# Kernel tuning notes

Hardware: AMD Instinct MI355X
Metric: run time of the kernel (lower is better)

## Reference

```python
import jax, jax.numpy as jnp
import numpy as np

HEADS = 16
NEG_INF = -1e30


def rel_shift(t):
    # t: [b, h, i, j] with i == j; Transformer-XL style relative shift
    b, h, i, j = t.shape
    t = jnp.pad(t, ((0, 0), (0, 0), (0, 0), (1, 0)))  # zero pad on last dim front
    t = t.reshape(b, h, j + 1, i)[:, :, 1:]
    return t.reshape(b, h, i, j)


def setup_inputs() -> dict:
    key = jax.random.key(0)
    ks = jax.random.split(key, 8)
    b, n, dim = 2, 2048, 1024
    d_head = dim // HEADS
    w = 0.02
    return {
        "x": jax.random.normal(ks[0], (b, n, dim), dtype=jnp.float32),
        "pos_emb": jax.random.normal(ks[1], (n, dim), dtype=jnp.float32),
        "Wq": jax.random.normal(ks[2], (dim, dim), dtype=jnp.float32) * w,
        "bq": jnp.zeros((dim,), dtype=jnp.float32),
        "Wkv": jax.random.normal(ks[3], (dim, 2 * dim), dtype=jnp.float32) * w,
        "bkv": jnp.zeros((2 * dim,), dtype=jnp.float32),
        "Wp": jax.random.normal(ks[4], (dim, d_head), dtype=jnp.float32) * w,
        "bp": jnp.zeros((d_head,), dtype=jnp.float32),
        "Wo": jax.random.normal(ks[5], (dim, dim), dtype=jnp.float32) * w,
        "bo": jnp.zeros((dim,), dtype=jnp.float32),
    }


def reference(x, pos_emb, Wq, bq, Wkv, bkv, Wp, bp, Wo, bo):
    b, n, dim = x.shape
    h = HEADS
    d = dim // h
    scale = d ** -0.5

    q = (x @ Wq + bq).reshape(b, n, h, d).transpose(0, 2, 1, 3)  # b h n d
    kv = x @ Wkv + bkv
    k, v = jnp.split(kv, 2, axis=-1)
    k = k.reshape(b, n, h, d).transpose(0, 2, 1, 3)
    v = v.reshape(b, n, h, d).transpose(0, 2, 1, 3)

    dots = jnp.einsum('bhid,bhjd->bhij', q, k) * scale

    # relative position bias
    p = pos_emb @ Wp + bp  # [n, d]
    pos_attn = jnp.einsum('bhid,jd->bhij', q, p) * scale
    dots = dots + rel_shift(pos_attn)

    # causal mask
    causal = jnp.triu(jnp.ones((n, n), dtype=bool), 1)
    dots = jnp.where(causal[None, None], NEG_INF, dots)

    attn = jax.nn.softmax(dots, axis=-1)
    out = jnp.einsum('bhij,bhjd->bhid', attn, v)
    out = out.transpose(0, 2, 1, 3).reshape(b, n, dim)
    return out @ Wo + bo
```

## Files before the change

kernel.cpp:

```cpp
#include <hip/hip_runtime.h>
#include <hip/hip_bf16.h>
#include <cstdint>
#include <cstddef>

#define SEQ_N 2048
#define DIM   1024
#define NHEAD 16
#define DH    64

typedef __bf16 bf16;
typedef __attribute__((ext_vector_type(8))) __bf16 bf16x8;
typedef __attribute__((ext_vector_type(4))) __bf16 bf16x4;
typedef __attribute__((ext_vector_type(4))) float f32x4;

__device__ __forceinline__ void gl_lds16(const bf16* g, bf16* l) {
    __builtin_amdgcn_global_load_lds(
        (const __attribute__((address_space(1))) unsigned int*)g,
        (__attribute__((address_space(3))) unsigned int*)l, 16, 0, 0);
}

__global__ __launch_bounds__(256) void prep_kernel(
    const float* __restrict__ x, const float* __restrict__ pos,
    const float* __restrict__ Wq, const float* __restrict__ Wkv,
    const float* __restrict__ Wo, const float* __restrict__ Wp,
    bf16* __restrict__ xb, bf16* __restrict__ posb,
    bf16* __restrict__ WqkvT, bf16* __restrict__ WoT, bf16* __restrict__ WpT)
{
    int bid = blockIdx.x;
    if (bid < 6144) {
        const int NX = 4096 * 1024;
        int i = (bid * 256 + threadIdx.x) * 4;
        if (i < NX) {
            float4 v = *(const float4*)&x[i];
            xb[i + 0] = (bf16)v.x; xb[i + 1] = (bf16)v.y;
            xb[i + 2] = (bf16)v.z; xb[i + 3] = (bf16)v.w;
        } else {
            int j = i - NX;
            float4 v = *(const float4*)&pos[j];
            posb[j + 0] = (bf16)v.x; posb[j + 1] = (bf16)v.y;
            posb[j + 2] = (bf16)v.z; posb[j + 3] = (bf16)v.w;
        }
        return;
    }
    __shared__ float t[32][33];
    bid -= 6144;
    const float* src; bf16* dst; int tidx, nx, N;
    if (bid < 1024)      { src = Wq;  dst = WqkvT;                       tidx = bid;        nx = 32; N = 1024; }
    else if (bid < 3072) { src = Wkv; dst = WqkvT + (size_t)1024 * 1024; tidx = bid - 1024; nx = 64; N = 2048; }
    else if (bid < 4096) { src = Wo;  dst = WoT;                         tidx = bid - 3072; nx = 32; N = 1024; }
    else                 { src = Wp;  dst = WpT;                         tidx = bid - 4096; nx = 2;  N = 64;   }
    int n0 = (tidx % nx) * 32, k0 = (tidx / nx) * 32;
    int tx = threadIdx.x & 31, ty = threadIdx.x >> 5;
    #pragma unroll
    for (int r = ty; r < 32; r += 8)
        t[r][tx] = src[(size_t)(k0 + r) * N + n0 + tx];
    __syncthreads();
    #pragma unroll
    for (int r = ty; r < 32; r += 8)
        dst[(size_t)(n0 + r) * 1024 + k0 + tx] = (bf16)t[tx][r];
}

__global__ __launch_bounds__(256) void qkvp_kernel(
    const bf16* __restrict__ xb, const bf16* __restrict__ WqkvT,
    const bf16* __restrict__ posb, const bf16* __restrict__ WpT,
    const float* __restrict__ bq, const float* __restrict__ bkv,
    const float* __restrict__ bp,
    bf16* __restrict__ qbuf, bf16* __restrict__ kbuf,
    bf16* __restrict__ vtbuf, bf16* __restrict__ pfrag)
{
    __shared__ __align__(16) bf16 sm[128 * 132];
    bf16* At = sm;
    bf16* Bt = sm + 128 * 64;
    const int tid = threadIdx.x, w = tid >> 6, lane = tid & 63;
    const int q = lane >> 4, ln15 = lane & 15;
    const int lr = lane >> 3, c_log = (lane & 7) ^ lr;
    const int bx = blockIdx.x, by = blockIdx.y;
    const int m0 = by * 128;

    if (bx == 24) {
        if (by >= 16) return;
        f32x4 acc[2][4] = {};
        for (int k0 = 0; k0 < 1024; k0 += 64) {
            __syncthreads();
            #pragma unroll
            for (int t = 0; t < 4; ++t)
                gl_lds16(&posb[(size_t)(m0 + 32 * w + 8 * t + lr) * 1024 + k0 + c_log * 8],
                         &At[(32 * w + 8 * t) * 64]);
            #pragma unroll
            for (int t = 0; t < 2; ++t)
                gl_lds16(&WpT[(size_t)(16 * w + 8 * t + lr) * 1024 + k0 + c_log * 8],
                         &Bt[(16 * w + 8 * t) * 64]);
            __syncthreads();
            bf16x8 bfr[2][4];
            #pragma unroll
            for (int ks = 0; ks < 2; ++ks)
                #pragma unroll
                for (int sn = 0; sn < 4; ++sn) {
                    int rb = 16 * sn + ln15;
                    bfr[ks][sn] = *(const bf16x8*)&Bt[(rb * 8 + ((4 * ks + q) ^ (rb & 7))) * 8];
                }
            #pragma unroll
            for (int sm2 = 0; sm2 < 2; ++sm2) {
                int ra = 32 * w + 16 * sm2 + ln15;
                #pragma unroll
                for (int ks = 0; ks < 2; ++ks) {
                    bf16x8 af = *(const bf16x8*)&At[(ra * 8 + ((4 * ks + q) ^ (ra & 7))) * 8];
                    #pragma unroll
                    for (int sn = 0; sn < 4; ++sn)
                        acc[sm2][sn] = __builtin_amdgcn_mfma_f32_16x16x32_bf16(
                            af, bfr[ks][sn], acc[sm2][sn], 0, 0, 0);
                }
            }
        }
        #pragma unroll
        for (int sm2 = 0; sm2 < 2; ++sm2)
            #pragma unroll
            for (int sn = 0; sn < 4; ++sn)
                #pragma unroll
                for (int r = 0; r < 4; ++r) {
                    int row = m0 + 32 * w + 16 * sm2 + 4 * q + r;
                    int d = 16 * sn + ln15;
                    int sb = row >> 4, lnp = row & 15;
                    int ks2 = d >> 5, qd = (d >> 3) & 3, e = d & 7;
                    pfrag[(((size_t)sb * 2 + ks2) * 64 + qd * 16 + lnp) * 8 + e] =
                        (bf16)(acc[sm2][sn][r] + bp[d]);
                }
        return;
    }

    const int n0 = bx * 128;
    const int wm = w >> 1, wn = w & 1;
    f32x4 acc[4][4] = {};

    for (int k0 = 0; k0 < 1024; k0 += 64) {
        __syncthreads();
        #pragma unroll
        for (int t = 0; t < 4; ++t) {
            int r = 32 * w + 8 * t + lr;
            gl_lds16(&xb[(size_t)(m0 + r) * 1024 + k0 + c_log * 8],
                     &At[(32 * w + 8 * t) * 64]);
            gl_lds16(&WqkvT[(size_t)(n0 + r) * 1024 + k0 + c_log * 8],
                     &Bt[(32 * w + 8 * t) * 64]);
        }
        __syncthreads();

        bf16x8 af[2][4], bfr[2][4];
        #pragma unroll
        for (int ks = 0; ks < 2; ++ks)
            #pragma unroll
            for (int s = 0; s < 4; ++s) {
                int ra = 64 * wm + 16 * s + ln15;
                af[ks][s]  = *(const bf16x8*)&At[(ra * 8 + ((4 * ks + q) ^ (ra & 7))) * 8];
                int rb = 64 * wn + 16 * s + ln15;
                bfr[ks][s] = *(const bf16x8*)&Bt[(rb * 8 + ((4 * ks + q) ^ (rb & 7))) * 8];
            }
        #pragma unroll
        for (int ks = 0; ks < 2; ++ks)
            #pragma unroll
            for (int si = 0; si < 4; ++si)
                #pragma unroll
                for (int sj = 0; sj < 4; ++sj)
                    acc[si][sj] = __builtin_amdgcn_mfma_f32_16x16x32_bf16(
                        af[ks][si], bfr[ks][sj], acc[si][sj], 0, 0, 0);
    }

    if (bx < 16) {
        #pragma unroll
        for (int si = 0; si < 4; ++si)
            #pragma unroll
            for (int sj = 0; sj < 4; ++sj)
                #pragma unroll
                for (int r = 0; r < 4; ++r) {
                    int row = m0 + 64 * wm + 16 * si + 4 * q + r;
                    int col = n0 + 64 * wn + 16 * sj + ln15;
                    float v = acc[si][sj][r] + (col < 1024 ? bq[col] : bkv[col - 1024]);
                    if (col < 1024) qbuf[(size_t)row * 1024 + col] = (bf16)v;
                    else            kbuf[(size_t)row * 1024 + (col - 1024)] = (bf16)v;
                }
    } else {
        __syncthreads();
        #pragma unroll
        for (int si = 0; si < 4; ++si)
            #pragma unroll
            for (int sj = 0; sj < 4; ++sj) {
                int dL = 64 * wn + 16 * sj + ln15;
                int tL = 64 * wm + 16 * si + 4 * q;
                float bias = bkv[1024 + (bx - 16) * 128 + dL];
                bf16x4 o4;
                #pragma unroll
                for (int r = 0; r < 4; ++r)
                    o4[r] = (bf16)(acc[si][sj][r] + bias);
                *(bf16x4*)&sm[dL * 132 + tL] = o4;
            }
        __syncthreads();
        const int b = m0 >> 11;
        const int t0 = m0 & 2047;
        const int h0 = (bx - 16) * 2;
        #pragma unroll
        for (int p = 0; p < 16; ++p) {
            int d = (tid >> 5) + 8 * p;
            int t = (tid & 31) * 4;
            bf16x4 v4 = *(const bf16x4*)&sm[d * 132 + t];
            int rowv = (b * NHEAD + h0 + (d >> 6)) * DH + (d & 63);
            *(bf16x4*)&vtbuf[(size_t)rowv * SEQ_N + t0 + t] = v4;
        }
    }
}

__global__ __launch_bounds__(256, 4) void attn_mfma_kernel(
    const bf16* __restrict__ qb,
    const bf16* __restrict__ kb,
    const bf16* __restrict__ vt,
    const bf16* __restrict__ pfrag,
    bf16* __restrict__ ob)
{
    const int f    = (int)blockIdx.x + ((int)blockIdx.y << 5);
    const int slot = f >> 3;
    const int bh   = ((f & 7) << 2) + (slot & 3);
    const int bi   = bh >> 4, hh = bh & 15;
    const int g    = (slot >> 2) & 7;
    const int pass = slot >> 5;
    const int qblk = (pass == 0) ? g
                   : (pass == 1) ? 15 - g
                   : (pass == 2) ? 16 + g
                   :               31 - g;
    const int i0 = qblk << 6;
    const int tid = threadIdx.x, w = tid >> 6, lane = tid & 63;
    const int q = lane >> 4, ln15 = lane & 15;
    const int lr = lane >> 3, c_log = (lane & 7) ^ lr;

    __shared__ __align__(16) bf16 smem[17664];
    bf16* Qs  = smem;
    bf16* S2L = smem + w * 1344;
    bf16* Ks  = smem + 5376;
    bf16* Vs  = smem + 9472;
    bf16* Pw  = smem + 13568 + w * 1024;

    const bf16* qbase = qb + ((size_t)(bi * SEQ_N + i0)) * DIM + hh * DH;
    const bf16* kbase = kb + ((size_t)bi * SEQ_N) * DIM + hh * DH;
    const bf16* vbase = vt + ((size_t)(bi * NHEAD + hh) * DH) * SEQ_N;

    #pragma unroll
    for (int t = 0; t < 2; ++t)
        gl_lds16(qbase + (size_t)(16 * w + 8 * t + lr) * DIM + c_log * 8,
                 &Qs[(16 * w + 8 * t) * 64]);
    __syncthreads();
    bf16x8 qf0, qf1;
    {
        int rq = 16 * w + ln15;
        qf0 = *(const bf16x8*)&Qs[(rq * 8 + ((q    ) ^ (rq & 7))) * 8];
        qf1 = *(const bf16x8*)&Qs[(rq * 8 + ((4 + q) ^ (rq & 7))) * 8];
    }
    __syncthreads();

    const int A0 = 127 - 4 * qblk - w;
    f32x4 s2r4;
    {
        bf16x8 f0 = *(const bf16x8*)&pfrag[(((size_t)A0 * 2 + 0) * 64 + lane) * 8];
        bf16x8 f1 = *(const bf16x8*)&pfrag[(((size_t)A0 * 2 + 1) * 64 + lane) * 8];
        f32x4 a = {0.f, 0.f, 0.f, 0.f};
        a = __builtin_amdgcn_mfma_f32_16x16x32_bf16(f0, qf0, a, 0, 0, 0);
        a = __builtin_amdgcn_mfma_f32_16x16x32_bf16(f1, qf1, a, 0, 0, 0);
        s2r4 = a;
    }

    float m_run = -1e30f, l_run = 0.f;
    f32x4 O_T[4] = {};

    for (int jt = 0; jt <= qblk; ++jt) {
        const int j0 = jt << 6;

        bf16x8 pfA[4][2];
        #pragma unroll
        for (int s = 1; s <= 4; ++s) {
            int sb = A0 + 4 * jt + s;
            if (sb > 127) sb = 127;
            pfA[s-1][0] = *(const bf16x8*)&pfrag[(((size_t)sb * 2 + 0) * 64 + lane) * 8];
            pfA[s-1][1] = *(const bf16x8*)&pfrag[(((size_t)sb * 2 + 1) * 64 + lane) * 8];
        }
        #pragma unroll
        for (int t = 0; t < 2; ++t) {
            int r = 16 * w + 8 * t + lr;
            gl_lds16(kbase + (size_t)(j0 + r) * DIM + c_log * 8,
                     &Ks[(16 * w + 8 * t) * 64]);
            gl_lds16(vbase + (size_t)r * SEQ_N + j0 + c_log * 8,
                     &Vs[(16 * w + 8 * t) * 64]);
        }

        f32x4 s2r[5];
        s2r[0] = s2r4;
        #pragma unroll
        for (int s = 1; s <= 4; ++s) {
            f32x4 a = {0.f, 0.f, 0.f, 0.f};
            a = __builtin_amdgcn_mfma_f32_16x16x32_bf16(pfA[s-1][0], qf0, a, 0, 0, 0);
            a = __builtin_amdgcn_mfma_f32_16x16x32_bf16(pfA[s-1][1], qf1, a, 0, 0, 0);
            s2r[s] = a;
        }
        s2r4 = s2r[4];
        #pragma unroll
        for (int s = 0; s < 5; ++s)
            #pragma unroll
            for (int r = 0; r < 4; ++r)
                S2L[ln15 * 84 + 16 * s + 4 * q + r] = (bf16)s2r[s][r];

        __syncthreads();

        float sv[4][4];
        #pragma unroll
        for (int sn = 0; sn < 4; ++sn) {
            int rk = 16 * sn + ln15;
            bf16x8 k0f = *(const bf16x8*)&Ks[(rk * 8 + ((q    ) ^ (rk & 7))) * 8];
            bf16x8 k1f = *(const bf16x8*)&Ks[(rk * 8 + ((4 + q) ^ (rk & 7))) * 8];
            f32x4 a = {0.f, 0.f, 0.f, 0.f};
            a = __builtin_amdgcn_mfma_f32_16x16x32_bf16(k0f, qf0, a, 0, 0, 0);
            a = __builtin_amdgcn_mfma_f32_16x16x32_bf16(k1f, qf1, a, 0, 0, 0);
            #pragma unroll
            for (int r = 0; r < 4; ++r) {
                int jl = 16 * sn + 4 * q + r;
                float b = (float)S2L[ln15 * 84 + 15 - ln15 + jl];
                sv[sn][r] = (a[r] + b) * 0.125f;
            }
        }
        if (jt == qblk) {
            #pragma unroll
            for (int sn = 0; sn < 4; ++sn)
                #pragma unroll
                for (int r = 0; r < 4; ++r)
                    if (16 * sn + 4 * q + r > 16 * w + ln15)
                        sv[sn][r] = -1e30f;
        }

        float mx = sv[0][0];
        #pragma unroll
        for (int sn = 0; sn < 4; ++sn)
            #pragma unroll
            for (int r = 0; r < 4; ++r)
                mx = fmaxf(mx, sv[sn][r]);
        mx = fmaxf(mx, __shfl_xor(mx, 16));
        mx = fmaxf(mx, __shfl_xor(mx, 32));
        const float mn = fmaxf(m_run, mx);
        float sum = 0.f;
        #pragma unroll
        for (int sn = 0; sn < 4; ++sn)
            #pragma unroll
            for (int r = 0; r < 4; ++r) {
                float e = __expf(sv[sn][r] - mn);
                sv[sn][r] = e;
                sum += e;
            }
        sum += __shfl_xor(sum, 16);
        sum += __shfl_xor(sum, 32);
        const float alpha = __expf(m_run - mn);
        l_run = l_run * alpha + sum;
        m_run = mn;

        #pragma unroll
        for (int sn = 0; sn < 4; ++sn)
            #pragma unroll
            for (int r = 0; r < 4; ++r) {
                int chunk = (2 * sn + (q >> 1)) ^ (ln15 & 7);
                Pw[ln15 * 64 + chunk * 8 + 4 * (q & 1) + r] = (bf16)sv[sn][r];
            }
        #pragma unroll
        for (int sd = 0; sd < 4; ++sd)
            #pragma unroll
            for (int r = 0; r < 4; ++r)
                O_T[sd][r] *= alpha;

        __builtin_amdgcn_s_waitcnt(0);

        #pragma unroll
        for (int ks = 0; ks < 2; ++ks) {
            bf16x8 pT = *(const bf16x8*)&Pw[ln15 * 64 + (((4 * ks + q) ^ (ln15 & 7))) * 8];
            #pragma unroll
            for (int sd = 0; sd < 4; ++sd) {
                int rv = 16 * sd + ln15;
                bf16x8 vf = *(const bf16x8*)&Vs[(rv * 8 + ((4 * ks + q) ^ (rv & 7))) * 8];
                O_T[sd] = __builtin_amdgcn_mfma_f32_16x16x32_bf16(vf, pT, O_T[sd], 0, 0, 0);
            }
        }
        __syncthreads();
    }

    const float inv = 1.0f / l_run;
    const size_t row = (size_t)bi * SEQ_N + i0 + 16 * w + ln15;
    #pragma unroll
    for (int sd = 0; sd < 4; ++sd) {
        bf16x4 o4;
        #pragma unroll
        for (int r = 0; r < 4; ++r)
            o4[r] = (bf16)(O_T[sd][r] * inv);
        *(bf16x4*)&ob[row * DIM + hh * DH + 16 * sd + 4 * q] = o4;
    }
}

__global__ __launch_bounds__(256) void outproj_kernel(
    const bf16* __restrict__ ab, const bf16* __restrict__ WoT,
    const float* __restrict__ bo, float* __restrict__ out)
{
    __shared__ __align__(16) bf16 At[128 * 64];
    __shared__ __align__(16) bf16 Bt[64 * 64];
    const int tid = threadIdx.x, w = tid >> 6, lane = tid & 63;
    const int q = lane >> 4, ln15 = lane & 15;
    const int lr = lane >> 3, c_log = (lane & 7) ^ lr;
    const int m0 = blockIdx.y * 128, n0 = blockIdx.x * 64;

    f32x4 acc[2][4] = {};
    for (int k0 = 0; k0 < 1024; k0 += 64) {
        __syncthreads();
        #pragma unroll
        for (int t = 0; t < 4; ++t)
            gl_lds16(&ab[(size_t)(m0 + 32 * w + 8 * t + lr) * 1024 + k0 + c_log * 8],
                     &At[(32 * w + 8 * t) * 64]);
        #pragma unroll
        for (int t = 0; t < 2; ++t)
            gl_lds16(&WoT[(size_t)(n0 + 16 * w + 8 * t + lr) * 1024 + k0 + c_log * 8],
                     &Bt[(16 * w + 8 * t) * 64]);
        __syncthreads();

        bf16x8 bfr[2][4];
        #pragma unroll
        for (int ks = 0; ks < 2; ++ks)
            #pragma unroll
            for (int sn = 0; sn < 4; ++sn) {
                int rb = 16 * sn + ln15;
                bfr[ks][sn] = *(const bf16x8*)&Bt[(rb * 8 + ((4 * ks + q) ^ (rb & 7))) * 8];
            }
        #pragma unroll
        for (int sm2 = 0; sm2 < 2; ++sm2) {
            int ra = 32 * w + 16 * sm2 + ln15;
            #pragma unroll
            for (int ks = 0; ks < 2; ++ks) {
                bf16x8 af = *(const bf16x8*)&At[(ra * 8 + ((4 * ks + q) ^ (ra & 7))) * 8];
                #pragma unroll
                for (int sn = 0; sn < 4; ++sn)
                    acc[sm2][sn] = __builtin_amdgcn_mfma_f32_16x16x32_bf16(
                        af, bfr[ks][sn], acc[sm2][sn], 0, 0, 0);
            }
        }
    }
    #pragma unroll
    for (int sm2 = 0; sm2 < 2; ++sm2)
        #pragma unroll
        for (int sn = 0; sn < 4; ++sn) {
            int col = n0 + 16 * sn + ln15;
            float bias = bo[col];
            #pragma unroll
            for (int r = 0; r < 4; ++r) {
                int row = m0 + 32 * w + 16 * sm2 + 4 * q + r;
                out[(size_t)row * 1024 + col] = acc[sm2][sn][r] + bias;
            }
        }
}

extern "C" void kernel_launch(void* const* d_in, const int* in_sizes, int n_in,
                              void* d_out, int out_size, void* d_ws, size_t ws_size,
                              hipStream_t stream)
{
    const float* x    = (const float*)d_in[0];
    const float* pos  = (const float*)d_in[1];
    const float* Wq   = (const float*)d_in[2];
    const float* bq   = (const float*)d_in[3];
    const float* Wkv  = (const float*)d_in[4];
    const float* bkv  = (const float*)d_in[5];
    const float* Wp   = (const float*)d_in[6];
    const float* bp   = (const float*)d_in[7];
    const float* Wo   = (const float*)d_in[8];
    const float* bo   = (const float*)d_in[9];
    float* out = (float*)d_out;

    const int M = 2 * SEQ_N;
    char* ws = (char*)d_ws;
    bf16* xb     = (bf16*)ws;  ws += (size_t)M * DIM * 2;
    bf16* posb   = (bf16*)ws;  ws += (size_t)SEQ_N * DIM * 2;
    bf16* WqkvT  = (bf16*)ws;  ws += (size_t)3072 * 1024 * 2;
    bf16* WoT    = (bf16*)ws;  ws += (size_t)DIM * DIM * 2;
    bf16* WpT    = (bf16*)ws;  ws += (size_t)DH * DIM * 2;
    bf16* qbuf   = (bf16*)ws;  ws += (size_t)M * DIM * 2;
    bf16* kbuf   = (bf16*)ws;  ws += (size_t)M * DIM * 2;
    bf16* vtbuf  = (bf16*)ws;  ws += (size_t)M * DIM * 2;
    bf16* pfrag  = (bf16*)ws;  ws += (size_t)512 * 1024;
    bf16* abuf   = (bf16*)ws;

    dim3 blk(256);
    prep_kernel<<<dim3(10304), blk, 0, stream>>>(
        x, pos, Wq, Wkv, Wo, Wp, xb, posb, WqkvT, WoT, WpT);

    qkvp_kernel<<<dim3(25, 32), blk, 0, stream>>>(
        xb, WqkvT, posb, WpT, bq, bkv, bp, qbuf, kbuf, vtbuf, pfrag);

    attn_mfma_kernel<<<dim3(32, 32), blk, 0, stream>>>(
        qbuf, kbuf, vtbuf, pfrag, abuf);

    outproj_kernel<<<dim3(16, 32), blk, 0, stream>>>(
        abuf, WoT, bo, out);
}
```

Measured before the change: 249.1 us.

## Software-pipeline K/V loads through registers and hoist positional-bias compute

Replaces the direct global-to-LDS loads of K/V with register prefetching one tile ahead, so the global load latency overlaps the current tile's compute. The positional S2 bias for the next tile is computed after the softmax instead of before the barrier. Q fragments are read straight from global memory, the exponentials switch to exp2 with a log2e-folded scale, and s_setprio is raised around the MFMA blocks. This adds register pressure and two barriers per iteration, and the S2L buffer is now written for the next tile inside the iteration, which depends on the placement of those barriers being correct.

```diff
diff --git a/kernel.cpp b/kernel.cpp
--- a/kernel.cpp
+++ b/kernel.cpp
@@ -230,28 +230,24 @@
     const int lr = lane >> 3, c_log = (lane & 7) ^ lr;
 
     __shared__ __align__(16) bf16 smem[17664];
-    bf16* Qs  = smem;
-    bf16* S2L = smem + w * 1344;
-    bf16* Ks  = smem + 5376;
-    bf16* Vs  = smem + 9472;
+    bf16* Ks  = smem;
+    bf16* Vs  = smem + 4096;
+    bf16* S2L = smem + 8192 + w * 1344;
     bf16* Pw  = smem + 13568 + w * 1024;
 
     const bf16* qbase = qb + ((size_t)(bi * SEQ_N + i0)) * DIM + hh * DH;
     const bf16* kbase = kb + ((size_t)bi * SEQ_N) * DIM + hh * DH;
     const bf16* vbase = vt + ((size_t)(bi * NHEAD + hh) * DH) * SEQ_N;
 
+    bf16x8 kreg[2], vreg[2];
     #pragma unroll
-    for (int t = 0; t < 2; ++t)
-        gl_lds16(qbase + (size_t)(16 * w + 8 * t + lr) * DIM + c_log * 8,
-                 &Qs[(16 * w + 8 * t) * 64]);
-    __syncthreads();
-    bf16x8 qf0, qf1;
-    {
-        int rq = 16 * w + ln15;
-        qf0 = *(const bf16x8*)&Qs[(rq * 8 + ((q    ) ^ (rq & 7))) * 8];
-        qf1 = *(const bf16x8*)&Qs[(rq * 8 + ((4 + q) ^ (rq & 7))) * 8];
-    }
-    __syncthreads();
+    for (int t = 0; t < 2; ++t) {
+        int r = 16 * w + 8 * t + lr;
+        kreg[t] = *(const bf16x8*)&kbase[(size_t)r * DIM + c_log * 8];
+        vreg[t] = *(const bf16x8*)&vbase[(size_t)r * SEQ_N + c_log * 8];
+    }
+    bf16x8 qf0 = *(const bf16x8*)&qbase[(size_t)(16 * w + ln15) * DIM + q * 8];
+    bf16x8 qf1 = *(const bf16x8*)&qbase[(size_t)(16 * w + ln15) * DIM + 32 + q * 8];
 
     const int A0 = 127 - 4 * qblk - w;
     f32x4 s2r4;
@@ -263,49 +259,63 @@
         a = __builtin_amdgcn_mfma_f32_16x16x32_bf16(f1, qf1, a, 0, 0, 0);
         s2r4 = a;
     }
-
+    {
+        f32x4 s2r[5];
+        s2r[0] = s2r4;
+        #pragma unroll
+        for (int s = 1; s <= 4; ++s) {
+            int sb = A0 + s; if (sb > 127) sb = 127;
+            bf16x8 f0 = *(const bf16x8*)&pfrag[(((size_t)sb * 2 + 0) * 64 + lane) * 8];
+            bf16x8 f1 = *(const bf16x8*)&pfrag[(((size_t)sb * 2 + 1) * 64 + lane) * 8];
+            f32x4 a = {0.f, 0.f, 0.f, 0.f};
+            a = __builtin_amdgcn_mfma_f32_16x16x32_bf16(f0, qf0, a, 0, 0, 0);
+            a = __builtin_amdgcn_mfma_f32_16x16x32_bf16(f1, qf1, a, 0, 0, 0);
+            s2r[s] = a;
+        }
+        s2r4 = s2r[4];
+        #pragma unroll
+        for (int s = 0; s < 5; ++s)
+            #pragma unroll
+            for (int r = 0; r < 4; ++r)
+                S2L[ln15 * 84 + 16 * s + 4 * q + r] = (bf16)s2r[s][r];
+    }
+    #pragma unroll
+    for (int t = 0; t < 2; ++t) {
+        *(bf16x8*)&Ks[(16 * w + 8 * t) * 64 + lane * 8] = kreg[t];
+        *(bf16x8*)&Vs[(16 * w + 8 * t) * 64 + lane * 8] = vreg[t];
+    }
+    asm volatile("s_waitcnt lgkmcnt(0)\n\ts_barrier" ::: "memory");
+    {
+        int jl = (qblk > 0) ? 1 : 0;
+        int j0n = jl << 6;
+        #pragma unroll
+        for (int t = 0; t < 2; ++t) {
+            int r = 16 * w + 8 * t + lr;
+            kreg[t] = *(const bf16x8*)&kbase[(size_t)(j0n + r) * DIM + c_log * 8];
+            vreg[t] = *(const bf16x8*)&vbase[(size_t)r * SEQ_N + j0n + c_log * 8];
+        }
+    }
+
+    const float SCL = 0.125f * 1.44269504088896341f;
     float m_run = -1e30f, l_run = 0.f;
     f32x4 O_T[4] = {};
 
-    for (int jt = 0; jt <= qblk; ++jt) {
-        const int j0 = jt << 6;
+    for (int jt = 0; ; ++jt) {
+        const bool doS2 = (jt < qblk);
 
         bf16x8 pfA[4][2];
-        #pragma unroll
-        for (int s = 1; s <= 4; ++s) {
-            int sb = A0 + 4 * jt + s;
-            if (sb > 127) sb = 127;
-            pfA[s-1][0] = *(const bf16x8*)&pfrag[(((size_t)sb * 2 + 0) * 64 + lane) * 8];
-            pfA[s-1][1] = *(const bf16x8*)&pfrag[(((size_t)sb * 2 + 1) * 64 + lane) * 8];
-        }
-        #pragma unroll
-        for (int t = 0; t < 2; ++t) {
-            int r = 16 * w + 8 * t + lr;
-            gl_lds16(kbase + (size_t)(j0 + r) * DIM + c_log * 8,
-                     &Ks[(16 * w + 8 * t) * 64]);
-            gl_lds16(vbase + (size_t)r * SEQ_N + j0 + c_log * 8,
-                     &Vs[(16 * w + 8 * t) * 64]);
-        }
-
-        f32x4 s2r[5];
-        s2r[0] = s2r4;
-        #pragma unroll
-        for (int s = 1; s <= 4; ++s) {
-            f32x4 a = {0.f, 0.f, 0.f, 0.f};
-            a = __builtin_amdgcn_mfma_f32_16x16x32_bf16(pfA[s-1][0], qf0, a, 0, 0, 0);
-            a = __builtin_amdgcn_mfma_f32_16x16x32_bf16(pfA[s-1][1], qf1, a, 0, 0, 0);
-            s2r[s] = a;
-        }
-        s2r4 = s2r[4];
-        #pragma unroll
-        for (int s = 0; s < 5; ++s)
-            #pragma unroll
-            for (int r = 0; r < 4; ++r)
-                S2L[ln15 * 84 + 16 * s + 4 * q + r] = (bf16)s2r[s][r];
-
-        __syncthreads();
+        if (doS2) {
+            #pragma unroll
+            for (int s = 1; s <= 4; ++s) {
+                int sb = A0 + 4 * (jt + 1) + s;
+                if (sb > 127) sb = 127;
+                pfA[s-1][0] = *(const bf16x8*)&pfrag[(((size_t)sb * 2 + 0) * 64 + lane) * 8];
+                pfA[s-1][1] = *(const bf16x8*)&pfrag[(((size_t)sb * 2 + 1) * 64 + lane) * 8];
+            }
+        }
 
         float sv[4][4];
+        __builtin_amdgcn_s_setprio(1);
         #pragma unroll
         for (int sn = 0; sn < 4; ++sn) {
             int rk = 16 * sn + ln15;
@@ -318,9 +328,10 @@
             for (int r = 0; r < 4; ++r) {
                 int jl = 16 * sn + 4 * q + r;
                 float b = (float)S2L[ln15 * 84 + 15 - ln15 + jl];
-                sv[sn][r] = (a[r] + b) * 0.125f;
-            }
-        }
+                sv[sn][r] = (a[r] + b) * SCL;
+            }
+        }
+        __builtin_amdgcn_s_setprio(0);
         if (jt == qblk) {
             #pragma unroll
             for (int sn = 0; sn < 4; ++sn)
@@ -344,15 +355,33 @@
         for (int sn = 0; sn < 4; ++sn)
             #pragma unroll
             for (int r = 0; r < 4; ++r) {
-                float e = __expf(sv[sn][r] - mn);
+                float e = exp2f(sv[sn][r] - mn);
                 sv[sn][r] = e;
                 sum += e;
             }
         sum += __shfl_xor(sum, 16);
         sum += __shfl_xor(sum, 32);
-        const float alpha = __expf(m_run - mn);
+        const float alpha = exp2f(m_run - mn);
         l_run = l_run * alpha + sum;
         m_run = mn;
+
+        if (doS2) {
+            f32x4 s2r[5];
+            s2r[0] = s2r4;
+            #pragma unroll
+            for (int s = 1; s <= 4; ++s) {
+                f32x4 a = {0.f, 0.f, 0.f, 0.f};
+                a = __builtin_amdgcn_mfma_f32_16x16x32_bf16(pfA[s-1][0], qf0, a, 0, 0, 0);
+                a = __builtin_amdgcn_mfma_f32_16x16x32_bf16(pfA[s-1][1], qf1, a, 0, 0, 0);
+                s2r[s] = a;
+            }
+            s2r4 = s2r[4];
+            #pragma unroll
+            for (int s = 0; s < 5; ++s)
+                #pragma unroll
+                for (int r = 0; r < 4; ++r)
+                    S2L[ln15 * 84 + 16 * s + 4 * q + r] = (bf16)s2r[s][r];
+        }
 
         #pragma unroll
         for (int sn = 0; sn < 4; ++sn)
@@ -367,8 +396,7 @@
             for (int r = 0; r < 4; ++r)
                 O_T[sd][r] *= alpha;
 
-        __builtin_amdgcn_s_waitcnt(0);
-
+        __builtin_amdgcn_s_setprio(1);
         #pragma unroll
         for (int ks = 0; ks < 2; ++ks) {
             bf16x8 pT = *(const bf16x8*)&Pw[ln15 * 64 + (((4 * ks + q) ^ (ln15 & 7))) * 8];
@@ -379,7 +407,30 @@
                 O_T[sd] = __builtin_amdgcn_mfma_f32_16x16x32_bf16(vf, pT, O_T[sd], 0, 0, 0);
             }
         }
-        __syncthreads();
+        __builtin_amdgcn_s_setprio(0);
+
+        if (jt == qblk) break;
+
+        asm volatile("s_waitcnt lgkmcnt(0)\n\ts_barrier" ::: "memory");
+
+        #pragma unroll
+        for (int t = 0; t < 2; ++t) {
+            *(bf16x8*)&Ks[(16 * w + 8 * t) * 64 + lane * 8] = kreg[t];
+            *(bf16x8*)&Vs[(16 * w + 8 * t) * 64 + lane * 8] = vreg[t];
+        }
+
+        {
+            int jl2 = (jt + 2 <= qblk) ? jt + 2 : qblk;
+            int j0n = jl2 << 6;
+            #pragma unroll
+            for (int t = 0; t < 2; ++t) {
+                int r = 16 * w + 8 * t + lr;
+                kreg[t] = *(const bf16x8*)&kbase[(size_t)(j0n + r) * DIM + c_log * 8];
+                vreg[t] = *(const bf16x8*)&vbase[(size_t)r * SEQ_N + j0n + c_log * 8];
+            }
+        }
+
+        asm volatile("s_waitcnt lgkmcnt(0)\n\ts_barrier" ::: "memory");
     }
 
     const float inv = 1.0f / l_run;
```

New measurement: 298.7 us. 1.2x slower.
